# Performance work log

Hardware: AMD Instinct MI355X
Metric: run time of the kernel (lower is better)

Reference implementation:

```python
import jax, jax.numpy as jnp
import numpy as np

B, S, D, H = 4, 2048, 1024, 16
HD = D // H


def setup_inputs() -> dict:
    key = jax.random.key(0)
    ks = jax.random.split(key, 5)
    scale = 1.0 / np.sqrt(D)
    return {
        "x": jax.random.normal(ks[0], (B, S, D), dtype=jnp.float32),
        "W_q": jax.random.normal(ks[1], (D, D), dtype=jnp.float32) * scale,
        "W_k": jax.random.normal(ks[2], (D, D), dtype=jnp.float32) * scale,
        "W_v": jax.random.normal(ks[3], (D, D), dtype=jnp.float32) * scale,
        "W_o": jax.random.normal(ks[4], (D, D), dtype=jnp.float32) * scale,
    }


def reference(x, W_q, W_k, W_v, W_o):
    # Linear with weight [out, in]: y = x @ W^T
    def proj(W):
        return jnp.einsum('bsd,ed->bshf', x, W.reshape(H, HD, D).transpose(0, 1, 2).reshape(D, D)) if False else (x @ W.T).reshape(B, S, H, HD).transpose(0, 2, 1, 3)

    q = proj(W_q)  # [B, H, S, HD]
    k = proj(W_k)
    v = proj(W_v)

    scores = jnp.einsum('bhqd,bhkd->bhqk', q, k) / jnp.sqrt(jnp.float32(HD))
    causal = jnp.triu(jnp.ones((S, S), dtype=bool), k=1)  # True above diagonal -> masked
    scores = jnp.where(causal, -jnp.inf, scores)
    probs = jax.nn.softmax(scores, axis=-1)
    out = jnp.einsum('bhqk,bhkd->bhqd', probs, v)  # [B, H, S, HD]
    out = out.transpose(0, 2, 1, 3).reshape(B, S, D)
    return out @ W_o.T
```

## Files before the change

### kernel.cpp

```cpp
#include <hip/hip_runtime.h>
#include <cstdint>
#include <cstddef>

typedef unsigned short u16;
typedef __attribute__((ext_vector_type(8))) short short8;
typedef __attribute__((ext_vector_type(4))) short short4v;
typedef __attribute__((ext_vector_type(8))) unsigned short ushort8v;
typedef __attribute__((ext_vector_type(4))) unsigned short ushort4v;
typedef __attribute__((ext_vector_type(4))) unsigned int uint4v;
typedef __attribute__((ext_vector_type(4))) float f32x4;

#define QSCALE 0.18033688011112042f
#define THR_L2 11.5417f


__device__ __forceinline__ u16 f2bf(float f) {
  unsigned int u = __builtin_bit_cast(unsigned int, f);
  u += 0x7FFFu + ((u >> 16) & 1u);
  return (u16)(u >> 16);
}

__device__ __forceinline__ void async16(const void* g, void* l) {
  __builtin_amdgcn_global_load_lds(
      (const __attribute__((address_space(1))) unsigned int*)g,
      (__attribute__((address_space(3))) unsigned int*)l, 16, 0, 0);
}

__device__ __forceinline__ float fmax3(float a, float b, float c) {
  float r;
  asm("v_max3_f32 %0, %1, %2, %3" : "=v"(r) : "v"(a), "v"(b), "v"(c));
  return r;
}

__device__ __forceinline__ unsigned int cvtpk(float lo, float hi) {
  unsigned int r;
  asm("v_cvt_pk_bf16_f32 %0, %1, %2" : "=v"(r) : "v"(lo), "v"(hi));
  return r;
}


__global__ void cvt_all(const float* __restrict__ x, const float* __restrict__ Wq,
                        const float* __restrict__ Wk, const float* __restrict__ Wv,
                        const float* __restrict__ Wo, u16* __restrict__ out) {
  const int bid = blockIdx.x;
  const float* src;
  int i;
  size_t doff;
  if (bid < 8192) {
    i = bid * 1024 + threadIdx.x * 4;
    src = x;
    doff = (size_t)i;
  } else {
    const int k = bid - 8192;
    const int wsel = k >> 10;
    i = (k & 1023) * 1024 + threadIdx.x * 4;
    src = (wsel == 0) ? Wq : (wsel == 1) ? Wk : (wsel == 2) ? Wv : Wo;
    doff = 8388608 + (size_t)wsel * 1048576 + i;
  }
  float4 v = *(const float4*)(src + i);
  ushort4v o;
  o[0] = f2bf(v.x); o[1] = f2bf(v.y); o[2] = f2bf(v.z); o[3] = f2bf(v.w);
  *(ushort4v*)(out + doff) = o;
}


template<int MODE>
__global__ __launch_bounds__(512, 4) void gemm_tb(
    const u16* __restrict__ A, const u16* __restrict__ Bw,
    void* __restrict__ Cout, int M, int N, int K)
{
  const int t = threadIdx.x;
  const int lane = t & 63, w = t >> 6;
  const int li = lane & 15, g = lane >> 4;
  const int wm = w >> 1, wn = w & 1;

  const int nx = gridDim.x;
  const int hwid = blockIdx.y * nx + blockIdx.x;
  const int cpx = (nx * gridDim.y) >> 3;
  const int lid = (hwid & 7) * cpx + (hwid >> 3);
  const int brow = (lid / nx) * 256, bcol = (lid % nx) * 128;

  __shared__ u16 As[3][256 * 32];
  __shared__ u16 Bs[3][128 * 32];

  f32x4 acc[4][4];
#pragma unroll
  for (int i = 0; i < 4; ++i)
#pragma unroll
    for (int j = 0; j < 4; ++j) acc[i][j] = f32x4{0.f, 0.f, 0.f, 0.f};

  auto STAGE = [&](int T) {
    const int b = T % 3;
    const int k0 = T * 32;
#pragma unroll
    for (int L = 0; L < 2; ++L) {
      const int f2 = t + 512 * L;
      const int row = f2 >> 2;
      const int cb = ((f2 & 3) * 16) ^ (((row >> 1) & 3) << 4);
      async16(A + (size_t)(brow + row) * K + k0 + (cb >> 1), &As[b][f2 * 8]);
    }
    const int rowb = t >> 2;
    const int cbb = ((t & 3) * 16) ^ (((rowb >> 1) & 3) << 4);
    async16(Bw + (size_t)(bcol + rowb) * K + k0 + (cbb >> 1), &Bs[b][t * 8]);
  };

  STAGE(0); STAGE(1);

  const int NT = K >> 5;
  const int ksw = (g * 8) ^ (((li >> 1) & 3) << 3);

#pragma unroll 1
  for (int T = 0; T < NT; ++T) {
    if (T < NT - 1) asm volatile("s_waitcnt vmcnt(3)" ::: "memory");
    else            asm volatile("s_waitcnt vmcnt(0)" ::: "memory");
    asm volatile("s_barrier" ::: "memory");
    const int b = T % 3;
    short8 af[4], bfr[4];
#pragma unroll
    for (int mt = 0; mt < 4; ++mt)
      af[mt] = *(const short8*)&As[b][(wm * 64 + mt * 16 + li) * 32 + ksw];
#pragma unroll
    for (int nt = 0; nt < 4; ++nt)
      bfr[nt] = *(const short8*)&Bs[b][(wn * 64 + nt * 16 + li) * 32 + ksw];

    if (T + 2 < NT) STAGE(T + 2);

    __builtin_amdgcn_s_setprio(1);
#pragma unroll
    for (int mt = 0; mt < 4; ++mt)
#pragma unroll
      for (int nt = 0; nt < 4; ++nt)
        acc[mt][nt] = __builtin_amdgcn_mfma_f32_16x16x32_bf16(af[mt], bfr[nt], acc[mt][nt], 0, 0, 0);
    __builtin_amdgcn_s_setprio(0);
  }

#pragma unroll
  for (int mt = 0; mt < 4; ++mt)
#pragma unroll
    for (int nt = 0; nt < 4; ++nt) {
      const int col = bcol + wn * 64 + nt * 16 + li;
      const int row0 = brow + wm * 64 + mt * 16 + g * 4;
      if (MODE == 1) {
#pragma unroll
        for (int r = 0; r < 4; ++r)
          ((float*)Cout)[(size_t)(row0 + r) * N + col] = acc[mt][nt][r];
      } else {
        const int which = col >> 10;
        const int c2 = col & 1023;
        const int h = c2 >> 6, hd = c2 & 63;
        const int bb = row0 >> 11, s0 = row0 & 2047;
        if (which == 2) {
          const int kv = s0 & 63;
          const int pos = (kv & 0x23) | ((kv & 0x10) >> 2) | ((kv & 0x0C) << 1);
          ushort4v st;
#pragma unroll
          for (int r = 0; r < 4; ++r) st[r] = f2bf(acc[mt][nt][r]);
          *(ushort4v*)((u16*)Cout + (size_t)3 * 8388608 +
                       (size_t)(bb * 16 + h) * 131072 + (size_t)hd * 2048 +
                       (s0 >> 6) * 64 + pos) = st;
        } else {
#pragma unroll
          for (int r = 0; r < 4; ++r) {
            float v = acc[mt][nt][r];
            if (which == 0) v *= QSCALE;
            ((u16*)Cout)[(size_t)which * 8388608 +
                         (((size_t)(bb * 16 + h) * 2048) + s0 + r) * 64 + hd] = f2bf(v);
          }
        }
      }
    }
}


__global__ __launch_bounds__(256, 2) void flash_attn9(
    const u16* __restrict__ Qp, const u16* __restrict__ Kp,
    const u16* __restrict__ VTp, u16* __restrict__ Oattn)
{
  const int hwid = blockIdx.x;
  const int lid = (hwid & 7) * 64 + (hwid >> 3);
  const int pr = lid & 7, bh = lid >> 3;

  const int t = threadIdx.x;
  const int lane = t & 63, w = t >> 6;
  const int li = lane & 15, g = lane >> 4;

  __shared__ u16 Kl[3][64 * 64];
  __shared__ u16 Vl[3][64 * 64];

  const size_t bh_off = (size_t)bh * (2048 * 64);
  const int tile0 = pr, tile1 = 15 - pr;
  const int njb0 = 2 * tile0 + 2;

  short8 qf0[2][2], qf1[2][2];
#pragma unroll
  for (int qs = 0; qs < 2; ++qs) {
    const u16* qp0 = Qp + bh_off + (size_t)(tile0 * 128 + qs * 64 + w * 16 + li) * 64 + g * 8;
    qf0[qs][0] = *(const short8*)qp0;
    qf0[qs][1] = *(const short8*)(qp0 + 32);
    const u16* qp1 = Qp + bh_off + (size_t)(tile1 * 128 + qs * 64 + w * 16 + li) * 64 + g * 8;
    qf1[qs][0] = *(const short8*)qp1;
    qf1[qs][1] = *(const short8*)(qp1 + 32);
  }
  short8 qc[2][2];
#pragma unroll
  for (int qs = 0; qs < 2; ++qs) { qc[qs][0] = qf0[qs][0]; qc[qs][1] = qf0[qs][1]; }

  int qbase = tile0 * 128;

  short8 onesf;
#pragma unroll
  for (int j = 0; j < 8; ++j) onesf[j] = (short)0x3F80;

  f32x4 o_acc[2][4];
  f32x4 osum[2];
#pragma unroll
  for (int qs = 0; qs < 2; ++qs) {
    osum[qs] = f32x4{0.f, 0.f, 0.f, 0.f};
#pragma unroll
    for (int i = 0; i < 4; ++i) o_acc[qs][i] = f32x4{0.f, 0.f, 0.f, 0.f};
  }
  float m_i[2] = {-1e30f, -1e30f};

  const int b = bh >> 4, h = bh & 15;
  const int ksw = (li & 7) << 3;

  auto STAGE = [&](int i, int s) {
    const int jb = (i < njb0) ? i : (i - njb0);
#pragma unroll
    for (int L = 0; L < 2; ++L) {
      const int f = t + 256 * L;
      const int kbyte = (f * 16) ^ (((f >> 3) & 7) << 4);
      async16(Kp + bh_off + (size_t)jb * 4096 + (kbyte >> 1),
              &Kl[s][(w * 64 + 256 * L) * 8]);
      const int vrow = f >> 3;
      const int vb = ((f & 7) * 16) ^ ((vrow & 7) << 4);
      async16(VTp + bh_off + (size_t)vrow * 2048 + jb * 64 + (vb >> 1),
              &Vl[s][(w * 64 + 256 * L) * 8]);
    }
  };

  auto WRITEO = [&]() {
#pragma unroll
    for (int qs = 0; qs < 2; ++qs) {
      const float inv_l = 1.f / osum[qs][0];
      const int qrow = qbase + qs * 64 + w * 16 + li;
      u16* op = Oattn + ((size_t)(b * 2048 + qrow)) * 1024 + h * 64;
#pragma unroll
      for (int dt = 0; dt < 4; ++dt) {
        ushort4v st;
#pragma unroll
        for (int r = 0; r < 4; ++r) st[r] = f2bf(o_acc[qs][dt][r] * inv_l);
        *(ushort4v*)(op + dt * 16 + g * 4) = st;
      }
    }
  };

  STAGE(0, 0);
  STAGE(1, 1);
  asm volatile("s_waitcnt vmcnt(4)" ::: "memory");
  __builtin_amdgcn_s_barrier();

#pragma unroll 1
  for (int i = 0; i < 34; ++i) {
    const int s = i % 3;
    if (i + 2 < 34) STAGE(i + 2, (i + 2) % 3);

    const int jb = (i < njb0) ? i : (i - njb0);
    const u16* __restrict__ Ks = &Kl[s][0];
    const u16* __restrict__ Vs = &Vl[s][0];

    f32x4 s_acc[2][4];
#pragma unroll
    for (int qs = 0; qs < 2; ++qs)
#pragma unroll
      for (int jt = 0; jt < 4; ++jt) s_acc[qs][jt] = f32x4{0.f, 0.f, 0.f, 0.f};
    __builtin_amdgcn_s_setprio(1);
#pragma unroll
    for (int kc = 0; kc < 2; ++kc)
#pragma unroll
      for (int jt = 0; jt < 4; ++jt) {
        short8 kf = *(const short8*)&Ks[(jt * 16 + li) * 64 + ((kc * 32 + g * 8) ^ ksw)];
        s_acc[0][jt] = __builtin_amdgcn_mfma_f32_16x16x32_bf16(kf, qc[0][kc], s_acc[0][jt], 0, 0, 0);
        s_acc[1][jt] = __builtin_amdgcn_mfma_f32_16x16x32_bf16(kf, qc[1][kc], s_acc[1][jt], 0, 0, 0);
      }
    __builtin_amdgcn_s_setprio(0);

    float mx[2];
    bool need = false;
#pragma unroll
    for (int qs = 0; qs < 2; ++qs) {
      if (jb * 64 + 63 > qbase + qs * 64 + w * 16) {
        const int tq = qbase + qs * 64 + w * 16 + li - jb * 64;
#pragma unroll
        for (int jt = 0; jt < 4; ++jt)
#pragma unroll
          for (int r = 0; r < 4; ++r)
            if (jt * 16 + g * 4 + r > tq) s_acc[qs][jt][r] = -1e30f;
      }
      float t0 = fmax3(s_acc[qs][0][0], s_acc[qs][0][1], s_acc[qs][0][2]);
      float t1 = fmax3(s_acc[qs][0][3], s_acc[qs][1][0], s_acc[qs][1][1]);
      float t2 = fmax3(s_acc[qs][1][2], s_acc[qs][1][3], s_acc[qs][2][0]);
      float t3 = fmax3(s_acc[qs][2][1], s_acc[qs][2][2], s_acc[qs][2][3]);
      float t4m = fmax3(s_acc[qs][3][0], s_acc[qs][3][1], s_acc[qs][3][2]);
      float m01 = fmax3(t0, t1, s_acc[qs][3][3]);
      float m23 = fmax3(t2, t3, t4m);
      float mm = fmaxf(m01, m23);
      mm = fmaxf(mm, __shfl_xor(mm, 16));
      mm = fmaxf(mm, __shfl_xor(mm, 32));
      mx[qs] = mm;
      need = need || (mm > m_i[qs] + THR_L2);
    }

    if (__any((int)need)) {
#pragma unroll
      for (int qs = 0; qs < 2; ++qs) {
        const float mn = fmaxf(m_i[qs], mx[qs]);
        const float corr = __builtin_amdgcn_exp2f(m_i[qs] - mn);
        osum[qs] *= corr;
#pragma unroll
        for (int dt = 0; dt < 4; ++dt) o_acc[qs][dt] *= corr;
        m_i[qs] = mn;
      }
    }

    short8 pf[2][2];
#pragma unroll
    for (int qs = 0; qs < 2; ++qs) {
      const float mi = m_i[qs];
#pragma unroll
      for (int jt = 0; jt < 4; ++jt)
#pragma unroll
        for (int r = 0; r < 4; ++r)
          s_acc[qs][jt][r] = __builtin_amdgcn_exp2f(s_acc[qs][jt][r] - mi);
#pragma unroll
      for (int kc = 0; kc < 2; ++kc) {
        uint4v u;
        u[0] = cvtpk(s_acc[qs][2 * kc][0], s_acc[qs][2 * kc][1]);
        u[1] = cvtpk(s_acc[qs][2 * kc][2], s_acc[qs][2 * kc][3]);
        u[2] = cvtpk(s_acc[qs][2 * kc + 1][0], s_acc[qs][2 * kc + 1][1]);
        u[3] = cvtpk(s_acc[qs][2 * kc + 1][2], s_acc[qs][2 * kc + 1][3]);
        pf[qs][kc] = __builtin_bit_cast(short8, u);
      }
    }

    __builtin_amdgcn_s_setprio(1);
#pragma unroll
    for (int kc = 0; kc < 2; ++kc) {
      osum[0] = __builtin_amdgcn_mfma_f32_16x16x32_bf16(onesf, pf[0][kc], osum[0], 0, 0, 0);
      osum[1] = __builtin_amdgcn_mfma_f32_16x16x32_bf16(onesf, pf[1][kc], osum[1], 0, 0, 0);
#pragma unroll
      for (int dt = 0; dt < 4; ++dt) {
        short8 vf = *(const short8*)&Vs[(dt * 16 + li) * 64 + ((kc * 32 + g * 8) ^ ksw)];
        o_acc[0][dt] = __builtin_amdgcn_mfma_f32_16x16x32_bf16(vf, pf[0][kc], o_acc[0][dt], 0, 0, 0);
        o_acc[1][dt] = __builtin_amdgcn_mfma_f32_16x16x32_bf16(vf, pf[1][kc], o_acc[1][dt], 0, 0, 0);
      }
    }
    __builtin_amdgcn_s_setprio(0);

    asm volatile("s_waitcnt lgkmcnt(0)" ::: "memory");
    if (i < 32) { asm volatile("s_waitcnt vmcnt(4)" ::: "memory"); }
    else        { asm volatile("s_waitcnt vmcnt(0)" ::: "memory"); }
    __builtin_amdgcn_s_barrier();

    if (i == njb0 - 1) {
      WRITEO();
      qbase = tile1 * 128;
#pragma unroll
      for (int qs = 0; qs < 2; ++qs) {
        qc[qs][0] = qf1[qs][0]; qc[qs][1] = qf1[qs][1];
        m_i[qs] = -1e30f;
        osum[qs] = f32x4{0.f, 0.f, 0.f, 0.f};
#pragma unroll
        for (int dt = 0; dt < 4; ++dt) o_acc[qs][dt] = f32x4{0.f, 0.f, 0.f, 0.f};
      }
    }
  }

  WRITEO();
}


extern "C" void kernel_launch(void* const* d_in, const int* in_sizes, int n_in,
                              void* d_out, int out_size, void* d_ws, size_t ws_size,
                              hipStream_t stream) {
  const float* x  = (const float*)d_in[0];
  const float* Wq = (const float*)d_in[1];
  const float* Wk = (const float*)d_in[2];
  const float* Wv = (const float*)d_in[3];
  const float* Wo = (const float*)d_in[4];

  const size_t NX = 8388608;
  const size_t NW = 1048576;

  u16* xb  = (u16*)d_ws;
  u16* wqb = xb + NX;
  u16* wob = wqb + 3 * NW;
  u16* Qb  = wob + NW;
  u16* Kb  = Qb + NX;
  u16* VTb = Qb + 3 * NX;
  u16* attnb = Qb + 2 * NX;

  cvt_all<<<12288, 256, 0, stream>>>(x, Wq, Wk, Wv, Wo, xb);

  gemm_tb<0><<<dim3(24, 32), 512, 0, stream>>>(xb, wqb, Qb, 8192, 3072, 1024);

  flash_attn9<<<512, 256, 0, stream>>>(Qb, Kb, VTb, attnb);

  gemm_tb<1><<<dim3(8, 32), 512, 0, stream>>>(attnb, wob, d_out, 8192, 1024, 1024);
}
```

Before: 157.1 us.

## Split paired causal tiles into separate blocks with double buffering and higher occupancy

The attention kernel no longer has each block process a balanced pair of query tiles (p and 15-p) in one 34-iteration loop. It now launches one block per query tile (1024 blocks), schedules heavy and light tiles in interleaved order per XCD, and cuts the LDS ring from triple to double buffering so launch bounds can allow 4 blocks per CU. This trades the fixed per-block work balance and deeper prefetch for more resident waves and finer-grained scheduling to hide latency. The load wait is now a full vmcnt(0) every iteration, which exposes more memory latency per block.

```diff
diff --git a/kernel.cpp b/kernel.cpp
--- a/kernel.cpp
+++ b/kernel.cpp
@@ -172,40 +172,36 @@
 }
 
 
-__global__ __launch_bounds__(256, 2) void flash_attn9(
+__global__ __launch_bounds__(256, 4) void flash_attn10(
     const u16* __restrict__ Qp, const u16* __restrict__ Kp,
     const u16* __restrict__ VTp, u16* __restrict__ Oattn)
 {
-  const int hwid = blockIdx.x;
-  const int lid = (hwid & 7) * 64 + (hwid >> 3);
-  const int pr = lid & 7, bh = lid >> 3;
+  const int id = blockIdx.x;
+  const int xcd = id & 7, r8 = id >> 3;
+  const int bh = xcd * 8 + (r8 >> 4);
+  const int e = r8 & 15;
+  const int p = (e & 1) ? 8 + (e >> 1) : 7 - (e >> 1);
+  const int qbase = p * 128;
+  const int njb = 2 * p + 2;
 
   const int t = threadIdx.x;
   const int lane = t & 63, w = t >> 6;
   const int li = lane & 15, g = lane >> 4;
 
-  __shared__ u16 Kl[3][64 * 64];
-  __shared__ u16 Vl[3][64 * 64];
+  __shared__ u16 Kl[2][64 * 64];
+  __shared__ u16 Vl[2][64 * 64];
 
   const size_t bh_off = (size_t)bh * (2048 * 64);
-  const int tile0 = pr, tile1 = 15 - pr;
-  const int njb0 = 2 * tile0 + 2;
-
-  short8 qf0[2][2], qf1[2][2];
+  const int b = bh >> 4, h = bh & 15;
+  const int ksw = (li & 7) << 3;
+
+  short8 qc[2][2];
 #pragma unroll
   for (int qs = 0; qs < 2; ++qs) {
-    const u16* qp0 = Qp + bh_off + (size_t)(tile0 * 128 + qs * 64 + w * 16 + li) * 64 + g * 8;
-    qf0[qs][0] = *(const short8*)qp0;
-    qf0[qs][1] = *(const short8*)(qp0 + 32);
-    const u16* qp1 = Qp + bh_off + (size_t)(tile1 * 128 + qs * 64 + w * 16 + li) * 64 + g * 8;
-    qf1[qs][0] = *(const short8*)qp1;
-    qf1[qs][1] = *(const short8*)(qp1 + 32);
-  }
-  short8 qc[2][2];
-#pragma unroll
-  for (int qs = 0; qs < 2; ++qs) { qc[qs][0] = qf0[qs][0]; qc[qs][1] = qf0[qs][1]; }
-
-  int qbase = tile0 * 128;
+    const u16* qp = Qp + bh_off + (size_t)(qbase + qs * 64 + w * 16 + li) * 64 + g * 8;
+    qc[qs][0] = *(const short8*)qp;
+    qc[qs][1] = *(const short8*)(qp + 32);
+  }
 
   short8 onesf;
 #pragma unroll
@@ -221,11 +217,7 @@
   }
   float m_i[2] = {-1e30f, -1e30f};
 
-  const int b = bh >> 4, h = bh & 15;
-  const int ksw = (li & 7) << 3;
-
-  auto STAGE = [&](int i, int s) {
-    const int jb = (i < njb0) ? i : (i - njb0);
+  auto STAGE = [&](int jb, int s) {
 #pragma unroll
     for (int L = 0; L < 2; ++L) {
       const int f = t + 256 * L;
@@ -239,33 +231,16 @@
     }
   };
 
-  auto WRITEO = [&]() {
-#pragma unroll
-    for (int qs = 0; qs < 2; ++qs) {
-      const float inv_l = 1.f / osum[qs][0];
-      const int qrow = qbase + qs * 64 + w * 16 + li;
-      u16* op = Oattn + ((size_t)(b * 2048 + qrow)) * 1024 + h * 64;
-#pragma unroll
-      for (int dt = 0; dt < 4; ++dt) {
-        ushort4v st;
-#pragma unroll
-        for (int r = 0; r < 4; ++r) st[r] = f2bf(o_acc[qs][dt][r] * inv_l);
-        *(ushort4v*)(op + dt * 16 + g * 4) = st;
-      }
-    }
-  };
-
   STAGE(0, 0);
-  STAGE(1, 1);
-  asm volatile("s_waitcnt vmcnt(4)" ::: "memory");
+  asm volatile("s_waitcnt vmcnt(0)" ::: "memory");
   __builtin_amdgcn_s_barrier();
 
 #pragma unroll 1
-  for (int i = 0; i < 34; ++i) {
-    const int s = i % 3;
-    if (i + 2 < 34) STAGE(i + 2, (i + 2) % 3);
-
-    const int jb = (i < njb0) ? i : (i - njb0);
+  for (int i = 0; i < njb; ++i) {
+    const int s = i & 1;
+    if (i + 1 < njb) STAGE(i + 1, (i + 1) & 1);
+
+    const int jb = i;
     const u16* __restrict__ Ks = &Kl[s][0];
     const u16* __restrict__ Vs = &Vl[s][0];
 
@@ -358,25 +333,23 @@
     __builtin_amdgcn_s_setprio(0);
 
     asm volatile("s_waitcnt lgkmcnt(0)" ::: "memory");
-    if (i < 32) { asm volatile("s_waitcnt vmcnt(4)" ::: "memory"); }
-    else        { asm volatile("s_waitcnt vmcnt(0)" ::: "memory"); }
+    asm volatile("s_waitcnt vmcnt(0)" ::: "memory");
     __builtin_amdgcn_s_barrier();
-
-    if (i == njb0 - 1) {
-      WRITEO();
-      qbase = tile1 * 128;
-#pragma unroll
-      for (int qs = 0; qs < 2; ++qs) {
-        qc[qs][0] = qf1[qs][0]; qc[qs][1] = qf1[qs][1];
-        m_i[qs] = -1e30f;
-        osum[qs] = f32x4{0.f, 0.f, 0.f, 0.f};
-#pragma unroll
-        for (int dt = 0; dt < 4; ++dt) o_acc[qs][dt] = f32x4{0.f, 0.f, 0.f, 0.f};
-      }
-    }
-  }
-
-  WRITEO();
+  }
+
+#pragma unroll
+  for (int qs = 0; qs < 2; ++qs) {
+    const float inv_l = 1.f / osum[qs][0];
+    const int qrow = qbase + qs * 64 + w * 16 + li;
+    u16* op = Oattn + ((size_t)(b * 2048 + qrow)) * 1024 + h * 64;
+#pragma unroll
+    for (int dt = 0; dt < 4; ++dt) {
+      ushort4v st;
+#pragma unroll
+      for (int r = 0; r < 4; ++r) st[r] = f2bf(o_acc[qs][dt][r] * inv_l);
+      *(ushort4v*)(op + dt * 16 + g * 4) = st;
+    }
+  }
 }
 
 
@@ -404,7 +377,7 @@
 
   gemm_tb<0><<<dim3(24, 32), 512, 0, stream>>>(xb, wqb, Qb, 8192, 3072, 1024);
 
-  flash_attn9<<<512, 256, 0, stream>>>(Qb, Kb, VTb, attnb);
+  flash_attn10<<<1024, 256, 0, stream>>>(Qb, Kb, VTb, attnb);
 
   gemm_tb<1><<<dim3(8, 32), 512, 0, stream>>>(attnb, wob, d_out, 8192, 1024, 1024);
 }
```

After: 177.3 us. +12.9%, slower.
